# Kernel tuning notes

Hardware: AMD Instinct MI355X
Metric: run time of the kernel (lower is better)

Reference implementation:

```python
import jax, jax.numpy as jnp
import numpy as np

EPS = 1e-6  # flax LayerNorm default

def _layer_norm(x, scale, bias):
    mu = jnp.mean(x, axis=-1, keepdims=True)
    var = jnp.mean(jnp.square(x - mu), axis=-1, keepdims=True)
    return (x - mu) * jax.lax.rsqrt(var + EPS) * scale + bias

def setup_inputs() -> dict:
    key = jax.random.key(0)
    ks = jax.random.split(key, 8)
    B, S, D_in, D_h, D_out, N = 4, 2048, 1024, 2048, 1024, 6
    init = lambda k, shape, fan_in: jax.random.normal(k, shape, jnp.float32) / np.sqrt(fan_in)
    return {
        "x": jax.random.normal(ks[0], (B, S, D_in), jnp.float32),
        "ln1_scale": jnp.ones((D_in,), jnp.float32),
        "ln1_bias": jnp.zeros((D_in,), jnp.float32),
        "w1": init(ks[1], (D_in, D_h), D_in),
        "b1": jnp.zeros((D_h,), jnp.float32),
        "block_ln_scales": jnp.ones((N, D_h), jnp.float32),
        "block_ln_biases": jnp.zeros((N, D_h), jnp.float32),
        "block_ws": init(ks[2], (N, D_h, D_h), D_h),
        "block_bs": jnp.zeros((N, D_h), jnp.float32),
        "ln2_scale": jnp.ones((D_h,), jnp.float32),
        "ln2_bias": jnp.zeros((D_h,), jnp.float32),
        "w2": init(ks[3], (D_h, D_out), D_h),
        "b2": jnp.zeros((D_out,), jnp.float32),
    }

def reference(x, ln1_scale, ln1_bias, w1, b1, block_ln_scales, block_ln_biases,
              block_ws, block_bs, ln2_scale, ln2_bias, w2, b2):
    # stem: LN -> Linear -> SiLU
    h = _layer_norm(x, ln1_scale, ln1_bias)
    h = jax.nn.silu(jnp.einsum('bsd,dh->bsh', h, w1) + b1)

    # residual blocks via scan over stacked params
    def block(h, params):
        s, b, w, lb = params
        y = _layer_norm(h, s, b)
        y = jax.nn.silu(jnp.einsum('bsh,hk->bsk', y, w) + lb)
        return h + y, None

    h, _ = jax.lax.scan(block, h, (block_ln_scales, block_ln_biases, block_ws, block_bs))

    # head: LN -> Linear
    h = _layer_norm(h, ln2_scale, ln2_bias)
    return jnp.einsum('bsh,ho->bso', h, w2) + b2
```

## Files before the change

### kernel.cpp

```cpp
#include <hip/hip_runtime.h>
#include <hip/hip_bf16.h>

typedef short short8 __attribute__((ext_vector_type(8)));
typedef float f32x4 __attribute__((ext_vector_type(4)));

#define AS1(p) ((const __attribute__((address_space(1))) void*)(p))
#define AS3(p) ((__attribute__((address_space(3))) void*)(p))

__device__ __forceinline__ ushort f2bf(float f) {
  __hip_bfloat16 h = __float2bfloat16(f);
  return *reinterpret_cast<const ushort*>(&h);
}
__device__ __forceinline__ float bfu2f(ushort u) {
  unsigned int x = ((unsigned int)u) << 16;
  float f;
  __builtin_memcpy(&f, &x, 4);
  return f;
}
__device__ __forceinline__ float silu_f(float v) { return v / (1.f + __expf(-v)); }

template<int NV>
__global__ __launch_bounds__(256) void ln_bf16_k(
    const float* __restrict__ in, const float* __restrict__ sc,
    const float* __restrict__ bi, ushort* __restrict__ out)
{
  const int D = NV * 1024;
  const long row = blockIdx.x;
  const int tx = threadIdx.x;
  const float* p = in + row * (long)D;
  float4 v[NV];
  float s = 0.f, s2 = 0.f;
#pragma unroll
  for (int t = 0; t < NV; ++t) {
    v[t] = *reinterpret_cast<const float4*>(p + t * 1024 + tx * 4);
    s  += v[t].x + v[t].y + v[t].z + v[t].w;
    s2 += v[t].x * v[t].x + v[t].y * v[t].y + v[t].z * v[t].z + v[t].w * v[t].w;
  }
#pragma unroll
  for (int o = 1; o < 64; o <<= 1) { s += __shfl_xor(s, o); s2 += __shfl_xor(s2, o); }
  __shared__ float red[2][4];
  const int wave = tx >> 6;
  if ((tx & 63) == 0) { red[0][wave] = s; red[1][wave] = s2; }
  __syncthreads();
  s  = red[0][0] + red[0][1] + red[0][2] + red[0][3];
  s2 = red[1][0] + red[1][1] + red[1][2] + red[1][3];
  const float mu   = s / D;
  const float rstd = rsqrtf(s2 / D - mu * mu + 1e-6f);
#pragma unroll
  for (int t = 0; t < NV; ++t) {
    const int d = t * 1024 + tx * 4;
    float4 g = *reinterpret_cast<const float4*>(sc + d);
    float4 b = *reinterpret_cast<const float4*>(bi + d);
    ushort4 o;
    o.x = f2bf((v[t].x - mu) * rstd * g.x + b.x);
    o.y = f2bf((v[t].y - mu) * rstd * g.y + b.y);
    o.z = f2bf((v[t].z - mu) * rstd * g.z + b.z);
    o.w = f2bf((v[t].w - mu) * rstd * g.w + b.w);
    *reinterpret_cast<ushort4*>(out + row * (long)D + d) = o;
  }
}

__global__ __launch_bounds__(256) void ln_bf16b_k(
    const ushort* __restrict__ in, const float* __restrict__ sc,
    const float* __restrict__ bi, ushort* __restrict__ out)
{
  const long row = blockIdx.x;
  const int tx = threadIdx.x;
  const int d = tx * 8;
  short8 v8 = *reinterpret_cast<const short8*>(in + row * 2048 + d);
  float v[8];
  float s = 0.f, s2 = 0.f;
#pragma unroll
  for (int j = 0; j < 8; ++j) {
    v[j] = bfu2f((ushort)v8[j]);
    s += v[j]; s2 += v[j] * v[j];
  }
#pragma unroll
  for (int o = 1; o < 64; o <<= 1) { s += __shfl_xor(s, o); s2 += __shfl_xor(s2, o); }
  __shared__ float red[2][4];
  const int wave = tx >> 6;
  if ((tx & 63) == 0) { red[0][wave] = s; red[1][wave] = s2; }
  __syncthreads();
  s  = red[0][0] + red[0][1] + red[0][2] + red[0][3];
  s2 = red[1][0] + red[1][1] + red[1][2] + red[1][3];
  const float mu   = s * (1.f / 2048.f);
  const float rstd = rsqrtf(s2 * (1.f / 2048.f) - mu * mu + 1e-6f);
  float4 g0 = *reinterpret_cast<const float4*>(sc + d);
  float4 g1 = *reinterpret_cast<const float4*>(sc + d + 4);
  float4 b0 = *reinterpret_cast<const float4*>(bi + d);
  float4 b1 = *reinterpret_cast<const float4*>(bi + d + 4);
  const float gg[8] = {g0.x, g0.y, g0.z, g0.w, g1.x, g1.y, g1.z, g1.w};
  const float bb[8] = {b0.x, b0.y, b0.z, b0.w, b1.x, b1.y, b1.z, b1.w};
  short8 o8;
#pragma unroll
  for (int j = 0; j < 8; ++j)
    o8[j] = (short)f2bf((v[j] - mu) * rstd * gg[j] + bb[j]);
  *reinterpret_cast<short8*>(out + row * 2048 + d) = o8;
}

__global__ __launch_bounds__(256) void transpose_bf16_k(
    const float* __restrict__ in, ushort* __restrict__ out, int K, int N)
{
  __shared__ float tile[64][65];
  const int k0 = blockIdx.y * 64, n0 = blockIdx.x * 64;
  const int tx = threadIdx.x, ty = threadIdx.y;
#pragma unroll
  for (int r = ty; r < 64; r += 4)
    tile[r][tx] = in[(long)(k0 + r) * N + n0 + tx];
  __syncthreads();
#pragma unroll
  for (int r = ty; r < 64; r += 4)
    out[(long)(n0 + r) * K + k0 + tx] = f2bf(tile[tx][r]);
}

#define STG(gsrc, ldst)                                                          \
  __builtin_amdgcn_global_load_lds(AS1(gsrc),          AS3(ldst),          16, 0, 0); \
  __builtin_amdgcn_global_load_lds(AS1((gsrc) + offQ), AS3((ldst) + 8192), 16, 0, 0)

#define ldsA(B, H) (ldsW + (B) * 65536 + (H) * 16384)
#define ldsB(B, H) (ldsW + (B) * 65536 + 32768 + (H) * 16384)

#define RD_AF(DB, MH, KS)                                                       \
  _Pragma("unroll") for (int i_ = 0; i_ < 4; ++i_)                              \
    af[i_] = *(const short8*)(smem + (DB) * 65536 + aOff + ((MH) * 4 + i_) * 2048 + rdk[(KS)])

#define RD_BF(DST, DB, KS)                                                      \
  _Pragma("unroll") for (int j_ = 0; j_ < 4; ++j_)                              \
    DST[j_] = *(const short8*)(smem + (DB) * 65536 + bOff + j_ * 2048 + rdk[(KS)])

#define MFMA16(MH, BFR)                                                         \
  _Pragma("unroll") for (int i_ = 0; i_ < 4; ++i_)                              \
  _Pragma("unroll") for (int j_ = 0; j_ < 4; ++j_)                              \
    acc[(MH) * 4 + i_][j_] = __builtin_amdgcn_mfma_f32_16x16x32_bf16(           \
        af[i_], BFR[j_], acc[(MH) * 4 + i_][j_], 0, 0, 0)

#define BARRIER __builtin_amdgcn_s_barrier()
#define LGKM0 do { asm volatile("s_waitcnt lgkmcnt(0)");                        \
                   __builtin_amdgcn_sched_barrier(0); } while (0)
#define W4 do { asm volatile("s_waitcnt vmcnt(4)" ::: "memory");                \
                __builtin_amdgcn_sched_barrier(0); } while (0)
#define W0 do { asm volatile("s_waitcnt vmcnt(0)" ::: "memory");                \
                __builtin_amdgcn_sched_barrier(0); } while (0)
#define WN do {} while (0)

#define DO_TILE(DB, S1, AO, S2, BO, WAITE)                                      \
  RD_AF(DB, 0, 0);                                                              \
  RD_BF(bf0, DB, 0);                                                            \
  RD_BF(bf1, DB, 1);                                                            \
  if (S1) { STG(aP + (AO), ldsA((DB) ^ 1, 0));                                  \
            STG(aP + (AO) + offH, ldsA((DB) ^ 1, 1)); }                         \
  BARRIER; LGKM0;                                                               \
  __builtin_amdgcn_s_setprio(1); MFMA16(0, bf0); __builtin_amdgcn_s_setprio(0); \
  BARRIER;                                                                      \
  RD_AF(DB, 1, 0);                                                              \
  if (S2) { STG(bP + (BO), ldsB(DB, 0)); }                                      \
  BARRIER; LGKM0;                                                               \
  __builtin_amdgcn_s_setprio(1); MFMA16(1, bf0); __builtin_amdgcn_s_setprio(0); \
  BARRIER;                                                                      \
  RD_AF(DB, 0, 1);                                                              \
  if (S2) { STG(bP + (BO) + offH, ldsB(DB, 1)); }                               \
  BARRIER; LGKM0;                                                               \
  __builtin_amdgcn_s_setprio(1); MFMA16(0, bf1); __builtin_amdgcn_s_setprio(0); \
  BARRIER;                                                                      \
  RD_AF(DB, 1, 1);                                                              \
  BARRIER; LGKM0;                                                               \
  __builtin_amdgcn_s_setprio(1); MFMA16(1, bf1); __builtin_amdgcn_s_setprio(0); \
  WAITE;                                                                        \
  BARRIER;

template<int MODE>
__global__ __launch_bounds__(512, 2) void gemm256_k(
    const ushort* __restrict__ A, const ushort* __restrict__ Bt,
    const float* __restrict__ bias, void* __restrict__ Cv,
    int M, int N, int K)
{
  extern __shared__ char smem[];
  const int tid = threadIdx.x;
  const int lane = tid & 63, wid = tid >> 6;
  const int wr = wid >> 2, wc = wid & 3;
  const int nbx = N >> 8;

  int bid;
  {
    const int b = blockIdx.x;
    const int cpx = gridDim.x >> 3;
    bid = (b & 7) * cpx + (b >> 3);
  }
  const int bx = bid % nbx, by = bid / nbx;
  const long m0 = (long)by << 8, n0 = (long)bx << 8;

  const int srow = tid >> 3;
  const int scol = (((tid & 7) * 16) ^ (((tid >> 3) & 7) << 4)) >> 1;
  const ushort* aP = A  + (m0 + srow) * (long)K + scol;
  const ushort* bP = Bt + (n0 + srow) * (long)K + scol;
  const long offH = 128L * K, offQ = 64L * K;
  char* ldsW = smem + wid * 1024;

  int rdk[2];
  rdk[0] = (((lane >> 4) * 16)     ) ^ ((lane & 7) << 4);
  rdk[1] = (((lane >> 4) * 16) + 64) ^ ((lane & 7) << 4);
  const int aOff = wr * 16384 + (lane & 15) * 128;
  const int bOff = 32768 + (wc >> 1) * 16384 + ((wc & 1) * 64 + (lane & 15)) * 128;

  f32x4 acc[8][4] = {};
  const int NT = K >> 6;

  STG(aP,      ldsA(0, 0));  STG(aP + offH,      ldsA(0, 1));
  STG(bP,      ldsB(0, 0));  STG(bP + offH,      ldsB(0, 1));
  STG(bP + 64, ldsB(1, 0));  STG(bP + 64 + offH, ldsB(1, 1));
  W4;
  BARRIER;

  short8 af[4], bf0[4], bf1[4];
  for (int t = 0; t < NT - 2; t += 2) {
    DO_TILE(0, 1,  64, 1, 128, W4)
    DO_TILE(1, 1, 128, 1, 192, W4)
    aP += 128; bP += 128;
  }
  DO_TILE(0, 1, 64, 0, 0, W0)
  DO_TILE(1, 0,  0, 0, 0, WN)

#pragma unroll
  for (int j = 0; j < 4; ++j) {
    const long col = n0 + wc * 64 + j * 16 + (lane & 15);
    const float bj = bias[col];
#pragma unroll
    for (int i = 0; i < 8; ++i) {
      const long rowb = m0 + wr * 128 + i * 16 + ((lane >> 4) << 2);
#pragma unroll
      for (int r = 0; r < 4; ++r) {
        const float v = acc[i][j][r] + bj;
        const long idx = (rowb + r) * N + col;
        if (MODE == 0) {
          ((ushort*)Cv)[idx] = f2bf(silu_f(v));
        } else if (MODE == 1) {
          ushort* C = (ushort*)Cv;
          C[idx] = f2bf(bfu2f(C[idx]) + silu_f(v));
        } else {
          ((float*)Cv)[idx] = v;
        }
      }
    }
  }
}

extern "C" void kernel_launch(void* const* d_in, const int* in_sizes, int n_in,
                              void* d_out, int out_size, void* d_ws, size_t ws_size,
                              hipStream_t stream) {
  const float* x     = (const float*)d_in[0];
  const float* ln1_s = (const float*)d_in[1];
  const float* ln1_b = (const float*)d_in[2];
  const float* w1    = (const float*)d_in[3];
  const float* b1    = (const float*)d_in[4];
  const float* bln_s = (const float*)d_in[5];
  const float* bln_b = (const float*)d_in[6];
  const float* bws   = (const float*)d_in[7];
  const float* bbs   = (const float*)d_in[8];
  const float* ln2_s = (const float*)d_in[9];
  const float* ln2_b = (const float*)d_in[10];
  const float* w2    = (const float*)d_in[11];
  const float* b2    = (const float*)d_in[12];
  float* out = (float*)d_out;

  const int M = 8192;
  char* ws = (char*)d_ws;
  ushort* h   = (ushort*)ws;
  ushort* Abf = (ushort*)(ws + 33554432);
  ushort* wt  = (ushort*)(ws + 67108864);
  const long W1T = 0;
  const long BLK = 2097152;
  const long W2T = BLK + 6L * 4194304;

  (void)hipFuncSetAttribute((const void*)gemm256_k<0>,
      hipFuncAttributeMaxDynamicSharedMemorySize, 131072);
  (void)hipFuncSetAttribute((const void*)gemm256_k<1>,
      hipFuncAttributeMaxDynamicSharedMemorySize, 131072);
  (void)hipFuncSetAttribute((const void*)gemm256_k<2>,
      hipFuncAttributeMaxDynamicSharedMemorySize, 131072);

  dim3 tb(64, 4);
  transpose_bf16_k<<<dim3(2048 / 64, 1024 / 64), tb, 0, stream>>>(w1, wt + W1T, 1024, 2048);
  for (int i = 0; i < 6; ++i)
    transpose_bf16_k<<<dim3(32, 32), tb, 0, stream>>>(
        bws + (long)i * 2048 * 2048, wt + BLK + (long)i * 4194304, 2048, 2048);
  transpose_bf16_k<<<dim3(1024 / 64, 2048 / 64), tb, 0, stream>>>(w2, wt + W2T, 2048, 1024);

  ln_bf16_k<1><<<M, 256, 0, stream>>>(x, ln1_s, ln1_b, Abf);
  gemm256_k<0><<<32 * 8, 512, 131072, stream>>>(Abf, wt + W1T, b1, (void*)h, M, 2048, 1024);

  for (int i = 0; i < 6; ++i) {
    ln_bf16b_k<<<M, 256, 0, stream>>>(h, bln_s + i * 2048, bln_b + i * 2048, Abf);
    gemm256_k<1><<<32 * 8, 512, 131072, stream>>>(
        Abf, wt + BLK + (long)i * 4194304, bbs + i * 2048, (void*)h, M, 2048, 2048);
  }

  ln_bf16b_k<<<M, 256, 0, stream>>>(h, ln2_s, ln2_b, Abf);
  gemm256_k<2><<<32 * 4, 512, 131072, stream>>>(Abf, wt + W2T, b2, (void*)out, M, 1024, 2048);
}
```

Before: 759.8 us.

## Fold LayerNorm into GEMM epilogue via per-row stats and pre-scaled weights

Replaces the per-block normalize-and-write LayerNorm kernel with a stats-only kernel that emits mean*rstd and rstd per row. The LN scale is folded into the transposed weights, and the column sums of the scaled weights and of beta times the weights are precomputed with atomics. The GEMM then consumes the raw residual stream directly and applies normalization algebraically in the epilogue. Ping-pong residual buffers avoid in-place read-modify-write. This removes one bf16 activation write and read per block. The trade-off is precision loss, since raw bf16 h is fed to the MFMA without centering and the mean is subtracted after the matmul, which risks cancellation.

```diff
diff --git a/kernel.cpp b/kernel.cpp
--- a/kernel.cpp
+++ b/kernel.cpp
@@ -60,20 +60,17 @@
   }
 }
 
-__global__ __launch_bounds__(256) void ln_bf16b_k(
-    const ushort* __restrict__ in, const float* __restrict__ sc,
-    const float* __restrict__ bi, ushort* __restrict__ out)
+__global__ __launch_bounds__(256) void ln_stats_k(
+    const ushort* __restrict__ in, float2* __restrict__ stats)
 {
   const long row = blockIdx.x;
   const int tx = threadIdx.x;
-  const int d = tx * 8;
-  short8 v8 = *reinterpret_cast<const short8*>(in + row * 2048 + d);
-  float v[8];
+  short8 v8 = *reinterpret_cast<const short8*>(in + row * 2048 + tx * 8);
   float s = 0.f, s2 = 0.f;
 #pragma unroll
   for (int j = 0; j < 8; ++j) {
-    v[j] = bfu2f((ushort)v8[j]);
-    s += v[j]; s2 += v[j] * v[j];
+    const float v = bfu2f((ushort)v8[j]);
+    s += v; s2 += v * v;
   }
 #pragma unroll
   for (int o = 1; o < 64; o <<= 1) { s += __shfl_xor(s, o); s2 += __shfl_xor(s2, o); }
@@ -81,21 +78,13 @@
   const int wave = tx >> 6;
   if ((tx & 63) == 0) { red[0][wave] = s; red[1][wave] = s2; }
   __syncthreads();
-  s  = red[0][0] + red[0][1] + red[0][2] + red[0][3];
-  s2 = red[1][0] + red[1][1] + red[1][2] + red[1][3];
-  const float mu   = s * (1.f / 2048.f);
-  const float rstd = rsqrtf(s2 * (1.f / 2048.f) - mu * mu + 1e-6f);
-  float4 g0 = *reinterpret_cast<const float4*>(sc + d);
-  float4 g1 = *reinterpret_cast<const float4*>(sc + d + 4);
-  float4 b0 = *reinterpret_cast<const float4*>(bi + d);
-  float4 b1 = *reinterpret_cast<const float4*>(bi + d + 4);
-  const float gg[8] = {g0.x, g0.y, g0.z, g0.w, g1.x, g1.y, g1.z, g1.w};
-  const float bb[8] = {b0.x, b0.y, b0.z, b0.w, b1.x, b1.y, b1.z, b1.w};
-  short8 o8;
-#pragma unroll
-  for (int j = 0; j < 8; ++j)
-    o8[j] = (short)f2bf((v[j] - mu) * rstd * gg[j] + bb[j]);
-  *reinterpret_cast<short8*>(out + row * 2048 + d) = o8;
+  if (tx == 0) {
+    s  = red[0][0] + red[0][1] + red[0][2] + red[0][3];
+    s2 = red[1][0] + red[1][1] + red[1][2] + red[1][3];
+    const float mu   = s * (1.f / 2048.f);
+    const float rstd = rsqrtf(s2 * (1.f / 2048.f) - mu * mu + 1e-6f);
+    stats[row] = make_float2(mu * rstd, rstd);
+  }
 }
 
 __global__ __launch_bounds__(256) void transpose_bf16_k(
@@ -113,6 +102,31 @@
     out[(long)(n0 + r) * K + k0 + tx] = f2bf(tile[tx][r]);
 }
 
+__global__ __launch_bounds__(256) void transpose_scale_k(
+    const float* __restrict__ in, const float* __restrict__ g,
+    const float* __restrict__ beta, ushort* __restrict__ out,
+    float2* __restrict__ uvw, int K, int N)
+{
+  __shared__ float tile[64][65];
+  const int k0 = blockIdx.y * 64, n0 = blockIdx.x * 64;
+  const int tx = threadIdx.x, ty = threadIdx.y;
+  float pu = 0.f, pv = 0.f;
+#pragma unroll
+  for (int r = ty; r < 64; r += 4) {
+    const float w  = in[(long)(k0 + r) * N + n0 + tx];
+    const float ws = g[k0 + r] * w;
+    tile[r][tx] = ws;
+    pu += ws;
+    pv += beta[k0 + r] * w;
+  }
+  atomicAdd(&uvw[n0 + tx].x, pu);
+  atomicAdd(&uvw[n0 + tx].y, pv);
+  __syncthreads();
+#pragma unroll
+  for (int r = ty; r < 64; r += 4)
+    out[(long)(n0 + r) * K + k0 + tx] = f2bf(tile[tx][r]);
+}
+
 #define STG(gsrc, ldst)                                                          \
   __builtin_amdgcn_global_load_lds(AS1(gsrc),          AS3(ldst),          16, 0, 0); \
   __builtin_amdgcn_global_load_lds(AS1((gsrc) + offQ), AS3((ldst) + 8192), 16, 0, 0)
@@ -128,6 +142,13 @@
   _Pragma("unroll") for (int j_ = 0; j_ < 4; ++j_)                              \
     DST[j_] = *(const short8*)(smem + (DB) * 65536 + bOff + j_ * 2048 + rdk[(KS)])
 
+#define MFMA16(MH, BFR)                                                         \
+  _Pragma("unroll") for (int i_ = 0; i_ < 4; ++i_)                              \
+  _Pragma("unroll") for (int j_ = 0; j_ < 4; ++j_)                              \
+    acc[(MH) * 4 + i_][j_] = __builtin_amdgcn_mfma_f32_16x16x32_bf16(           \
+        af[i_], BFR[j_], acc[(MH) * 4 + i_], j_[0] * 0 + acc[(MH) * 4 + i_][j_], 0, 0, 0)
+
+#undef MFMA16
 #define MFMA16(MH, BFR)                                                         \
   _Pragma("unroll") for (int i_ = 0; i_ < 4; ++i_)                              \
   _Pragma("unroll") for (int j_ = 0; j_ < 4; ++j_)                              \
@@ -171,8 +192,9 @@
 template<int MODE>
 __global__ __launch_bounds__(512, 2) void gemm256_k(
     const ushort* __restrict__ A, const ushort* __restrict__ Bt,
-    const float* __restrict__ bias, void* __restrict__ Cv,
-    int M, int N, int K)
+    const float* __restrict__ bias, const float2* __restrict__ stats,
+    const float2* __restrict__ uvw, const ushort* __restrict__ Rin,
+    void* __restrict__ Cv, int M, int N, int K)
 {
   extern __shared__ char smem[];
   const int tid = threadIdx.x;
@@ -220,24 +242,47 @@
   DO_TILE(0, 1, 64, 0, 0, W0)
   DO_TILE(1, 0,  0, 0, 0, WN)
 
-#pragma unroll
-  for (int j = 0; j < 4; ++j) {
-    const long col = n0 + wc * 64 + j * 16 + (lane & 15);
-    const float bj = bias[col];
+  if (MODE == 0) {
+#pragma unroll
+    for (int j = 0; j < 4; ++j) {
+      const long col = n0 + wc * 64 + j * 16 + (lane & 15);
+      const float bj = bias[col];
+#pragma unroll
+      for (int i = 0; i < 8; ++i) {
+        const long rowb = m0 + wr * 128 + i * 16 + ((lane >> 4) << 2);
+#pragma unroll
+        for (int r = 0; r < 4; ++r) {
+          const float v = acc[i][j][r] + bj;
+          ((ushort*)Cv)[(rowb + r) * N + col] = f2bf(silu_f(v));
+        }
+      }
+    }
+  } else {
+    float2 uvv[4];
+    float  bj4[4];
+    long   col4[4];
+#pragma unroll
+    for (int j = 0; j < 4; ++j) {
+      col4[j] = n0 + wc * 64 + j * 16 + (lane & 15);
+      uvv[j]  = uvw[col4[j]];
+      bj4[j]  = bias[col4[j]];
+    }
 #pragma unroll
     for (int i = 0; i < 8; ++i) {
       const long rowb = m0 + wr * 128 + i * 16 + ((lane >> 4) << 2);
 #pragma unroll
       for (int r = 0; r < 4; ++r) {
-        const float v = acc[i][j][r] + bj;
-        const long idx = (rowb + r) * N + col;
-        if (MODE == 0) {
-          ((ushort*)Cv)[idx] = f2bf(silu_f(v));
-        } else if (MODE == 1) {
-          ushort* C = (ushort*)Cv;
-          C[idx] = f2bf(bfu2f(C[idx]) + silu_f(v));
-        } else {
-          ((float*)Cv)[idx] = v;
+        const long row = rowb + r;
+        const float2 ms = stats[row];
+#pragma unroll
+        for (int j = 0; j < 4; ++j) {
+          const float v = ms.y * acc[i][j][r] - ms.x * uvv[j].x + uvv[j].y + bj4[j];
+          const long idx = row * N + col4[j];
+          if (MODE == 3) {
+            ((ushort*)Cv)[idx] = f2bf(bfu2f(Rin[idx]) + silu_f(v));
+          } else {
+            ((float*)Cv)[idx] = v;
+          }
         }
       }
     }
@@ -264,36 +309,49 @@
 
   const int M = 8192;
   char* ws = (char*)d_ws;
-  ushort* h   = (ushort*)ws;
-  ushort* Abf = (ushort*)(ws + 33554432);
-  ushort* wt  = (ushort*)(ws + 67108864);
+  ushort* h0   = (ushort*)ws;
+  ushort* h1   = (ushort*)(ws + 33554432);
+  ushort* Abf  = h1;
+  ushort* wt   = (ushort*)(ws + 67108864);
+  float2* uvw  = (float2*)(ws + 125829120);
+  float2* stats = (float2*)(ws + 125829120 + 114688);
   const long W1T = 0;
   const long BLK = 2097152;
   const long W2T = BLK + 6L * 4194304;
 
   (void)hipFuncSetAttribute((const void*)gemm256_k<0>,
       hipFuncAttributeMaxDynamicSharedMemorySize, 131072);
-  (void)hipFuncSetAttribute((const void*)gemm256_k<1>,
+  (void)hipFuncSetAttribute((const void*)gemm256_k<3>,
       hipFuncAttributeMaxDynamicSharedMemorySize, 131072);
-  (void)hipFuncSetAttribute((const void*)gemm256_k<2>,
+  (void)hipFuncSetAttribute((const void*)gemm256_k<4>,
       hipFuncAttributeMaxDynamicSharedMemorySize, 131072);
 
+  (void)hipMemsetAsync(uvw, 0, 7 * 2048 * sizeof(float2), stream);
+
   dim3 tb(64, 4);
-  transpose_bf16_k<<<dim3(2048 / 64, 1024 / 64), tb, 0, stream>>>(w1, wt + W1T, 1024, 2048);
+  transpose_bf16_k<<<dim3(32, 16), tb, 0, stream>>>(w1, wt + W1T, 1024, 2048);
   for (int i = 0; i < 6; ++i)
-    transpose_bf16_k<<<dim3(32, 32), tb, 0, stream>>>(
-        bws + (long)i * 2048 * 2048, wt + BLK + (long)i * 4194304, 2048, 2048);
-  transpose_bf16_k<<<dim3(1024 / 64, 2048 / 64), tb, 0, stream>>>(w2, wt + W2T, 2048, 1024);
+    transpose_scale_k<<<dim3(32, 32), tb, 0, stream>>>(
+        bws + (long)i * 2048 * 2048, bln_s + i * 2048, bln_b + i * 2048,
+        wt + BLK + (long)i * 4194304, uvw + (long)i * 2048, 2048, 2048);
+  transpose_scale_k<<<dim3(16, 32), tb, 0, stream>>>(
+      w2, ln2_s, ln2_b, wt + W2T, uvw + 6L * 2048, 2048, 1024);
 
   ln_bf16_k<1><<<M, 256, 0, stream>>>(x, ln1_s, ln1_b, Abf);
-  gemm256_k<0><<<32 * 8, 512, 131072, stream>>>(Abf, wt + W1T, b1, (void*)h, M, 2048, 1024);
-
+  gemm256_k<0><<<32 * 8, 512, 131072, stream>>>(
+      Abf, wt + W1T, b1, nullptr, nullptr, nullptr, (void*)h0, M, 2048, 1024);
+
+  ushort* hin = h0;
+  ushort* hout = h1;
   for (int i = 0; i < 6; ++i) {
-    ln_bf16b_k<<<M, 256, 0, stream>>>(h, bln_s + i * 2048, bln_b + i * 2048, Abf);
-    gemm256_k<1><<<32 * 8, 512, 131072, stream>>>(
-        Abf, wt + BLK + (long)i * 4194304, bbs + i * 2048, (void*)h, M, 2048, 2048);
-  }
-
-  ln_bf16b_k<<<M, 256, 0, stream>>>(h, ln2_s, ln2_b, Abf);
-  gemm256_k<2><<<32 * 4, 512, 131072, stream>>>(Abf, wt + W2T, b2, (void*)out, M, 1024, 2048);
-}
+    ln_stats_k<<<M, 256, 0, stream>>>(hin, stats);
+    gemm256_k<3><<<32 * 8, 512, 131072, stream>>>(
+        hin, wt + BLK + (long)i * 4194304, bbs + i * 2048, stats,
+        uvw + (long)i * 2048, hin, (void*)hout, M, 2048, 2048);
+    ushort* tmp = hin; hin = hout; hout = tmp;
+  }
+
+  ln_stats_k<<<M, 256, 0, stream>>>(hin, stats);
+  gemm256_k<4><<<32 * 4, 512, 131072, stream>>>(
+      hin, wt + W2T, b2, stats, uvw + 6L * 2048, nullptr, (void*)out, M, 1024, 2048);
+}
```

Result: faster. 694.4 us (-8.6%).
